# Kernel optimization log

Hardware: AMD Instinct MI355X
Metric: run time of the kernel (lower is better)

Reference implementation:

```python
import jax, jax.numpy as jnp
import numpy as np

HEADS = 8
DIM_HEAD = 64
QUERY_DIM = 512
INNER_DIM = HEADS * DIM_HEAD  # 512
SCALE = DIM_HEAD ** -0.5


def setup_inputs() -> dict:
    key = jax.random.key(0)
    k0, k1, k2, k3, k4 = jax.random.split(key, 5)
    B, S = 4, 2048
    hidden_states = jax.random.normal(k0, (B, S, QUERY_DIM), dtype=jnp.float32)
    init = lambda k, fin, fout: jax.random.normal(k, (fin, fout), dtype=jnp.float32) / np.sqrt(fin)
    return {
        "hidden_states": hidden_states,
        "Wq": init(k1, QUERY_DIM, INNER_DIM),
        "Wk": init(k2, QUERY_DIM, INNER_DIM),
        "Wv": init(k3, QUERY_DIM, INNER_DIM),
        "Wo": init(k4, INNER_DIM, QUERY_DIM),
    }


def _split_heads(x):
    # [B, S, H*D] -> [B, H, S, D]
    B, S, _ = x.shape
    return x.reshape(B, S, HEADS, DIM_HEAD).transpose(0, 2, 1, 3)


def reference(hidden_states, Wq, Wk, Wv, Wo):
    q = _split_heads(hidden_states @ Wq)
    k = _split_heads(hidden_states @ Wk)
    v = _split_heads(hidden_states @ Wv)
    # scores: [B, H, S, S]
    scores = jnp.einsum("bhid,bhjd->bhij", q, k) * SCALE
    attn = jax.nn.softmax(scores, axis=-1)
    out = jnp.einsum("bhij,bhjd->bhid", attn, v)  # [B, H, S, D]
    B, H, S, D = out.shape
    out = out.transpose(0, 2, 1, 3).reshape(B, S, H * D)
    return out @ Wo
```

## Files before the change

kernel.cpp:

```cpp
#include <hip/hip_runtime.h>
#include <hip/hip_bf16.h>

typedef __bf16 bf16;
typedef __attribute__((ext_vector_type(8))) __bf16 bf16x8;
typedef __attribute__((ext_vector_type(4))) float f32x4;

#define SEQ   2048
#define HEADS 8
#define DHEAD 64
#define CDIM  512
#define MROWS 8192
#define SCALE 0.125f

__global__ __launch_bounds__(256) void k_cvt_hs(const float* __restrict__ in,
                                                bf16* __restrict__ out) {
    int idx = blockIdx.x * 256 + threadIdx.x;
    const float4* in4 = reinterpret_cast<const float4*>(in);
    float4 a = in4[idx * 2], b = in4[idx * 2 + 1];
    bf16x8 o;
    o[0] = (bf16)a.x; o[1] = (bf16)a.y; o[2] = (bf16)a.z; o[3] = (bf16)a.w;
    o[4] = (bf16)b.x; o[5] = (bf16)b.y; o[6] = (bf16)b.z; o[7] = (bf16)b.w;
    reinterpret_cast<bf16x8*>(out)[idx] = o;
}

__global__ __launch_bounds__(256) void k_wtrans(const float* __restrict__ w0,
                                                const float* __restrict__ w1,
                                                const float* __restrict__ w2,
                                                const float* __restrict__ w3,
                                                bf16* __restrict__ wt) {
    const float* w = blockIdx.z == 0 ? w0 : blockIdx.z == 1 ? w1 : blockIdx.z == 2 ? w2 : w3;
    bf16* out = wt + (size_t)blockIdx.z * CDIM * CDIM;
    __shared__ bf16 tile[64][65];
    const int t = threadIdx.x;
    const int r0 = blockIdx.x * 64, c0 = blockIdx.y * 64;
    const int r = t >> 2, cc = (t & 3) * 16;
    const float4* src = reinterpret_cast<const float4*>(w + (size_t)(r0 + r) * CDIM + c0 + cc);
#pragma unroll
    for (int v = 0; v < 4; ++v) {
        float4 f = src[v];
        tile[r][cc + v * 4 + 0] = (bf16)f.x;
        tile[r][cc + v * 4 + 1] = (bf16)f.y;
        tile[r][cc + v * 4 + 2] = (bf16)f.z;
        tile[r][cc + v * 4 + 3] = (bf16)f.w;
    }
    __syncthreads();
    bf16x8 o0, o1;
#pragma unroll
    for (int j = 0; j < 8; ++j) { o0[j] = tile[cc + j][r]; o1[j] = tile[cc + 8 + j][r]; }
    bf16* dst = out + (size_t)(c0 + r) * CDIM + r0 + cc;
    *reinterpret_cast<bf16x8*>(dst) = o0;
    *reinterpret_cast<bf16x8*>(dst + 8) = o1;
}

__global__ __launch_bounds__(256) void k_gemm_qkv(const bf16* __restrict__ A,
                                                  const bf16* __restrict__ Wt,
                                                  bf16* __restrict__ Qb,
                                                  bf16* __restrict__ Kb,
                                                  bf16* __restrict__ Vb) {
    __shared__ __align__(16) bf16 As[128 * 32];
    __shared__ __align__(16) bf16 Bs[128 * 32];
    const int t = threadIdx.x, lane = t & 63, wid = t >> 6;
    const int wr = wid >> 1, wc = wid & 1;
    const int g = (lane >> 4) & 3, q = lane & 15;
    const int m0 = blockIdx.x * 128, n0 = blockIdx.y * 128;
    const bf16* Bmat = Wt + (size_t)blockIdx.z * CDIM * CDIM;
    f32x4 acc[4][4] = {};
    const int sr = t >> 1, sc = (t & 1) * 16;
    for (int kt = 0; kt < 16; ++kt) {
        const int k0 = kt * 32;
        const bf16x8* a_src = reinterpret_cast<const bf16x8*>(A + (size_t)(m0 + sr) * CDIM + k0 + sc);
        const bf16x8* b_src = reinterpret_cast<const bf16x8*>(Bmat + (size_t)(n0 + sr) * CDIM + k0 + sc);
        bf16x8 av0 = a_src[0], av1 = a_src[1];
        bf16x8 bv0 = b_src[0], bv1 = b_src[1];
        __syncthreads();
        *reinterpret_cast<bf16x8*>(&As[sr * 32 + sc]) = av0;
        *reinterpret_cast<bf16x8*>(&As[sr * 32 + sc + 8]) = av1;
        *reinterpret_cast<bf16x8*>(&Bs[sr * 32 + sc]) = bv0;
        *reinterpret_cast<bf16x8*>(&Bs[sr * 32 + sc + 8]) = bv1;
        __syncthreads();
        bf16x8 af[4], bfv[4];
#pragma unroll
        for (int m = 0; m < 4; ++m)
            af[m] = *reinterpret_cast<const bf16x8*>(&As[(wr * 64 + m * 16 + q) * 32 + g * 8]);
#pragma unroll
        for (int n = 0; n < 4; ++n)
            bfv[n] = *reinterpret_cast<const bf16x8*>(&Bs[(wc * 64 + n * 16 + q) * 32 + g * 8]);
#pragma unroll
        for (int m = 0; m < 4; ++m)
#pragma unroll
            for (int n = 0; n < 4; ++n)
                acc[m][n] = __builtin_amdgcn_mfma_f32_16x16x32_bf16(af[m], bfv[n], acc[m][n], 0, 0, 0);
    }
    bf16* outp = blockIdx.z == 0 ? Qb : (blockIdx.z == 1 ? Kb : Vb);
#pragma unroll
    for (int m = 0; m < 4; ++m) {
        const int rbase = m0 + wr * 64 + m * 16 + g * 4;
#pragma unroll
        for (int i = 0; i < 4; ++i) {
            const int row = rbase + i;
            const int b = row >> 11, s = row & 2047;
#pragma unroll
            for (int n = 0; n < 4; ++n) {
                const int col = n0 + wc * 64 + n * 16 + q;
                const int h = col >> 6, d = col & 63;
                outp[((((size_t)b * HEADS + h) * SEQ + s) << 6) + d] = (bf16)acc[m][n][i];
            }
        }
    }
}

__global__ __launch_bounds__(256) void k_vtrans(const bf16* __restrict__ V,
                                                bf16* __restrict__ Vt) {
    __shared__ bf16 tile[64][65];
    const int t = threadIdx.x;
    const int s0 = blockIdx.x * 64;
    const size_t bh = blockIdx.y;
    const int r = t >> 2, cc = (t & 3) * 16;
    const bf16x8* src = reinterpret_cast<const bf16x8*>(V + (bh * SEQ + s0 + r) * DHEAD + cc);
    bf16x8 v0 = src[0], v1 = src[1];
#pragma unroll
    for (int j = 0; j < 8; ++j) { tile[r][cc + j] = v0[j]; tile[r][cc + 8 + j] = v1[j]; }
    __syncthreads();
    bf16x8 o0, o1;
#pragma unroll
    for (int j = 0; j < 8; ++j) { o0[j] = tile[cc + j][r]; o1[j] = tile[cc + 8 + j][r]; }
    bf16* dst = Vt + (bh * DHEAD + r) * SEQ + s0 + cc;
    *reinterpret_cast<bf16x8*>(dst) = o0;
    *reinterpret_cast<bf16x8*>(dst + 8) = o1;
}

__global__ __launch_bounds__(256) void k_attn(const bf16* __restrict__ Qg,
                                              const bf16* __restrict__ Kg,
                                              const bf16* __restrict__ Vtg,
                                              bf16* __restrict__ Og) {
    __shared__ __align__(16) bf16 K_lds[64 * 72];
    __shared__ __align__(16) bf16 Vt_lds[64 * 72];
    __shared__ __align__(16) bf16 P_lds[4][16 * 72];
    const int t = threadIdx.x, lane = t & 63, wid = t >> 6;
    const int g = (lane >> 4) & 3, q = lane & 15;
    const size_t bh = blockIdx.y;
    const int q0 = blockIdx.x * 64 + wid * 16;
    const int b = (int)(bh >> 3), h = (int)(bh & 7);

    bf16x8 qf[2];
#pragma unroll
    for (int ks = 0; ks < 2; ++ks)
        qf[ks] = *reinterpret_cast<const bf16x8*>(Qg + (bh * SEQ + q0 + q) * DHEAD + ks * 32 + g * 8);

    f32x4 accO[4] = {};
    float m_run = -1e30f, l_run = 0.f;
    const int sr = t >> 2, scc = (t & 3) * 16;

    for (int kt = 0; kt < 32; ++kt) {
        const int kv0 = kt * 64;
        const bf16x8* ksrc = reinterpret_cast<const bf16x8*>(Kg + (bh * SEQ + kv0 + sr) * DHEAD + scc);
        const bf16x8* vsrc = reinterpret_cast<const bf16x8*>(Vtg + (bh * DHEAD + sr) * SEQ + kv0 + scc);
        bf16x8 kva = ksrc[0], kvb = ksrc[1];
        bf16x8 vva = vsrc[0], vvb = vsrc[1];
        __syncthreads();
        *reinterpret_cast<bf16x8*>(&K_lds[sr * 72 + scc]) = kva;
        *reinterpret_cast<bf16x8*>(&K_lds[sr * 72 + scc + 8]) = kvb;
        *reinterpret_cast<bf16x8*>(&Vt_lds[sr * 72 + scc]) = vva;
        *reinterpret_cast<bf16x8*>(&Vt_lds[sr * 72 + scc + 8]) = vvb;
        __syncthreads();

        f32x4 st[4] = {};
#pragma unroll
        for (int ks = 0; ks < 2; ++ks) {
            bf16x8 qk = qf[ks];
#pragma unroll
            for (int m = 0; m < 4; ++m) {
                bf16x8 kf = *reinterpret_cast<const bf16x8*>(&K_lds[(m * 16 + q) * 72 + ks * 32 + g * 8]);
                st[m] = __builtin_amdgcn_mfma_f32_16x16x32_bf16(kf, qk, st[m], 0, 0, 0);
            }
        }

        float sc[4][4];
        float tmax = -1e30f;
#pragma unroll
        for (int m = 0; m < 4; ++m)
#pragma unroll
            for (int i = 0; i < 4; ++i) {
                sc[m][i] = st[m][i] * SCALE;
                tmax = fmaxf(tmax, sc[m][i]);
            }
        tmax = fmaxf(tmax, __shfl_xor(tmax, 16));
        tmax = fmaxf(tmax, __shfl_xor(tmax, 32));
        const float mnew = fmaxf(m_run, tmax);
        const float alpha = __expf(m_run - mnew);
        float psum = 0.f;
#pragma unroll
        for (int m = 0; m < 4; ++m)
#pragma unroll
            for (int i = 0; i < 4; ++i) {
                float p = __expf(sc[m][i] - mnew);
                psum += p;
                P_lds[wid][q * 72 + m * 16 + g * 4 + i] = (bf16)p;
            }
        psum += __shfl_xor(psum, 16);
        psum += __shfl_xor(psum, 32);
        l_run = l_run * alpha + psum;
        m_run = mnew;
#pragma unroll
        for (int m = 0; m < 4; ++m)
#pragma unroll
            for (int i = 0; i < 4; ++i) accO[m][i] *= alpha;

#pragma unroll
        for (int ks = 0; ks < 2; ++ks) {
            bf16x8 pb = *reinterpret_cast<const bf16x8*>(&P_lds[wid][q * 72 + ks * 32 + g * 8]);
#pragma unroll
            for (int m = 0; m < 4; ++m) {
                bf16x8 vf = *reinterpret_cast<const bf16x8*>(&Vt_lds[(m * 16 + q) * 72 + ks * 32 + g * 8]);
                accO[m] = __builtin_amdgcn_mfma_f32_16x16x32_bf16(vf, pb, accO[m], 0, 0, 0);
            }
        }
    }

    const float inv = 1.0f / l_run;
#pragma unroll
    for (int m = 0; m < 4; ++m)
#pragma unroll
        for (int i = 0; i < 4; ++i) {
            const int d = m * 16 + g * 4 + i;
            Og[((size_t)b * SEQ + q0 + q) * (HEADS * DHEAD) + h * DHEAD + d] = (bf16)(accO[m][i] * inv);
        }
}

__global__ __launch_bounds__(256) void k_gemm_o(const bf16* __restrict__ A,
                                                const bf16* __restrict__ Bt,
                                                float* __restrict__ out) {
    __shared__ __align__(16) bf16 As[128 * 32];
    __shared__ __align__(16) bf16 Bs[128 * 32];
    const int t = threadIdx.x, lane = t & 63, wid = t >> 6;
    const int wr = wid >> 1, wc = wid & 1;
    const int g = (lane >> 4) & 3, q = lane & 15;
    const int m0 = blockIdx.x * 128, n0 = blockIdx.y * 128;
    f32x4 acc[4][4] = {};
    const int sr = t >> 1, sc = (t & 1) * 16;
    for (int kt = 0; kt < 16; ++kt) {
        const int k0 = kt * 32;
        const bf16x8* a_src = reinterpret_cast<const bf16x8*>(A + (size_t)(m0 + sr) * CDIM + k0 + sc);
        const bf16x8* b_src = reinterpret_cast<const bf16x8*>(Bt + (size_t)(n0 + sr) * CDIM + k0 + sc);
        bf16x8 av0 = a_src[0], av1 = a_src[1];
        bf16x8 bv0 = b_src[0], bv1 = b_src[1];
        __syncthreads();
        *reinterpret_cast<bf16x8*>(&As[sr * 32 + sc]) = av0;
        *reinterpret_cast<bf16x8*>(&As[sr * 32 + sc + 8]) = av1;
        *reinterpret_cast<bf16x8*>(&Bs[sr * 32 + sc]) = bv0;
        *reinterpret_cast<bf16x8*>(&Bs[sr * 32 + sc + 8]) = bv1;
        __syncthreads();
        bf16x8 af[4], bfv[4];
#pragma unroll
        for (int m = 0; m < 4; ++m)
            af[m] = *reinterpret_cast<const bf16x8*>(&As[(wr * 64 + m * 16 + q) * 32 + g * 8]);
#pragma unroll
        for (int n = 0; n < 4; ++n)
            bfv[n] = *reinterpret_cast<const bf16x8*>(&Bs[(wc * 64 + n * 16 + q) * 32 + g * 8]);
#pragma unroll
        for (int m = 0; m < 4; ++m)
#pragma unroll
            for (int n = 0; n < 4; ++n)
                acc[m][n] = __builtin_amdgcn_mfma_f32_16x16x32_bf16(af[m], bfv[n], acc[m][n], 0, 0, 0);
    }
#pragma unroll
    for (int m = 0; m < 4; ++m) {
        const int rbase = m0 + wr * 64 + m * 16 + g * 4;
#pragma unroll
        for (int i = 0; i < 4; ++i) {
            const int row = rbase + i;
#pragma unroll
            for (int n = 0; n < 4; ++n) {
                const int col = n0 + wc * 64 + n * 16 + q;
                out[(size_t)row * CDIM + col] = acc[m][n][i];
            }
        }
    }
}

extern "C" void kernel_launch(void* const* d_in, const int* in_sizes, int n_in,
                              void* d_out, int out_size, void* d_ws, size_t ws_size,
                              hipStream_t stream) {
    const float* hs = (const float*)d_in[0];
    const float* Wq = (const float*)d_in[1];
    const float* Wk = (const float*)d_in[2];
    const float* Wv = (const float*)d_in[3];
    const float* Wo = (const float*)d_in[4];
    float* out = (float*)d_out;

    bf16* hs_bf = (bf16*)d_ws;
    bf16* wt    = hs_bf + 4194304;
    bf16* Qb    = wt + 4 * 262144;
    bf16* Kb    = Qb + 4194304;
    bf16* Vb    = Kb + 4194304;
    bf16* Vt    = Vb + 4194304;
    bf16* Ob    = Vt + 4194304;

    k_cvt_hs<<<2048, 256, 0, stream>>>(hs, hs_bf);
    k_wtrans<<<dim3(8, 8, 4), 256, 0, stream>>>(Wq, Wk, Wv, Wo, wt);
    k_gemm_qkv<<<dim3(64, 4, 3), 256, 0, stream>>>(hs_bf, wt, Qb, Kb, Vb);
    k_vtrans<<<dim3(32, 32), 256, 0, stream>>>(Vb, Vt);
    k_attn<<<dim3(32, 32), 256, 0, stream>>>(Qb, Kb, Vt, Ob);
    k_gemm_o<<<dim3(64, 4), 256, 0, stream>>>(Ob, wt + 3 * 262144, out);
}
```

Measured before the change: 188.8 us.

## Rewrite QKV, attention and output kernels with async LDS loads and fragment layouts

```diff
diff --git a/kernel.cpp b/kernel.cpp
--- a/kernel.cpp
+++ b/kernel.cpp
@@ -1,16 +1,31 @@
 #include <hip/hip_runtime.h>
 #include <hip/hip_bf16.h>
+#include <stdint.h>
 
 typedef __bf16 bf16;
 typedef __attribute__((ext_vector_type(8))) __bf16 bf16x8;
 typedef __attribute__((ext_vector_type(4))) float f32x4;
+typedef __attribute__((ext_vector_type(16))) float f32x16;
 
 #define SEQ   2048
 #define HEADS 8
-#define DHEAD 64
 #define CDIM  512
-#define MROWS 8192
-#define SCALE 0.125f
+#define C2      0.18033688011112043f
+#define THR_RAW 44.3614f
+
+__device__ __forceinline__ void glds16(const bf16* g, bf16* l) {
+    __builtin_amdgcn_global_load_lds((const __attribute__((address_space(1))) void*)g,
+                                     (__attribute__((address_space(3))) void*)l, 16, 0, 0);
+}
+__device__ __forceinline__ uint32_t pk_bf16(float a, float b) {
+    uint32_t r; asm("v_cvt_pk_bf16_f32 %0, %1, %2" : "=v"(r) : "v"(a), "v"(b)); return r;
+}
+__device__ __forceinline__ void pl_swap(uint32_t &a, uint32_t &b) {
+    asm("v_permlane32_swap_b32 %0, %1" : "+v"(a), "+v"(b));
+}
+__device__ __forceinline__ void wait_vm4() { asm volatile("s_waitcnt vmcnt(4)" ::: "memory"); }
+__device__ __forceinline__ void wait_vm3() { asm volatile("s_waitcnt vmcnt(3)" ::: "memory"); }
+__device__ __forceinline__ void wait_vm0() { asm volatile("s_waitcnt vmcnt(0)" ::: "memory"); }
 
 __global__ __launch_bounds__(256) void k_cvt_hs(const float* __restrict__ in,
                                                 bf16* __restrict__ out) {
@@ -54,226 +69,262 @@
 
 __global__ __launch_bounds__(256) void k_gemm_qkv(const bf16* __restrict__ A,
                                                   const bf16* __restrict__ Wt,
-                                                  bf16* __restrict__ Qb,
-                                                  bf16* __restrict__ Kb,
-                                                  bf16* __restrict__ Vb) {
-    __shared__ __align__(16) bf16 As[128 * 32];
-    __shared__ __align__(16) bf16 Bs[128 * 32];
+                                                  bf16* __restrict__ Qg,
+                                                  bf16* __restrict__ Kf,
+                                                  bf16* __restrict__ Vf) {
+    __shared__ __align__(16) bf16 As[2][4096];
+    __shared__ __align__(16) bf16 Bs[2][4096];
+    const int id = blockIdx.x;
+    const int swz = (id & 7) * 96 + (id >> 3);
+    const int mt = swz & 63, r2 = swz >> 6;
+    const int nt = r2 & 3, z = r2 >> 2;
+    const int m0 = mt * 128, n0 = nt * 128;
     const int t = threadIdx.x, lane = t & 63, wid = t >> 6;
     const int wr = wid >> 1, wc = wid & 1;
-    const int g = (lane >> 4) & 3, q = lane & 15;
-    const int m0 = blockIdx.x * 128, n0 = blockIdx.y * 128;
-    const bf16* Bmat = Wt + (size_t)blockIdx.z * CDIM * CDIM;
+    const int q = lane & 15, g = lane >> 4;
+    const bf16* Bmat = Wt + (size_t)z * 262144;
+    const int srow = lane >> 2, scol = (lane & 3) * 8;
+
+    auto stage = [&](int buf, int kt) {
+        const int k0 = kt * 32;
+        const bf16* a0 = A + (size_t)(m0 + wid * 32 + srow) * CDIM + k0 + scol;
+        glds16(a0,             &As[buf][wid * 1024]);
+        glds16(a0 + 16 * CDIM, &As[buf][wid * 1024 + 512]);
+        const bf16* b0 = Bmat + (size_t)(n0 + wid * 32 + srow) * CDIM + k0 + scol;
+        glds16(b0,             &Bs[buf][wid * 1024]);
+        glds16(b0 + 16 * CDIM, &Bs[buf][wid * 1024 + 512]);
+    };
+
     f32x4 acc[4][4] = {};
-    const int sr = t >> 1, sc = (t & 1) * 16;
+    stage(0, 0);
     for (int kt = 0; kt < 16; ++kt) {
-        const int k0 = kt * 32;
-        const bf16x8* a_src = reinterpret_cast<const bf16x8*>(A + (size_t)(m0 + sr) * CDIM + k0 + sc);
-        const bf16x8* b_src = reinterpret_cast<const bf16x8*>(Bmat + (size_t)(n0 + sr) * CDIM + k0 + sc);
-        bf16x8 av0 = a_src[0], av1 = a_src[1];
-        bf16x8 bv0 = b_src[0], bv1 = b_src[1];
-        __syncthreads();
-        *reinterpret_cast<bf16x8*>(&As[sr * 32 + sc]) = av0;
-        *reinterpret_cast<bf16x8*>(&As[sr * 32 + sc + 8]) = av1;
-        *reinterpret_cast<bf16x8*>(&Bs[sr * 32 + sc]) = bv0;
-        *reinterpret_cast<bf16x8*>(&Bs[sr * 32 + sc + 8]) = bv1;
+        const int cur = kt & 1;
+        if (kt < 15) { stage(cur ^ 1, kt + 1); wait_vm4(); } else wait_vm0();
         __syncthreads();
         bf16x8 af[4], bfv[4];
 #pragma unroll
         for (int m = 0; m < 4; ++m)
-            af[m] = *reinterpret_cast<const bf16x8*>(&As[(wr * 64 + m * 16 + q) * 32 + g * 8]);
+            af[m] = *(const bf16x8*)&As[cur][(wr * 64 + m * 16 + q) * 32 + g * 8];
 #pragma unroll
         for (int n = 0; n < 4; ++n)
-            bfv[n] = *reinterpret_cast<const bf16x8*>(&Bs[(wc * 64 + n * 16 + q) * 32 + g * 8]);
+            bfv[n] = *(const bf16x8*)&Bs[cur][(wc * 64 + n * 16 + q) * 32 + g * 8];
 #pragma unroll
         for (int m = 0; m < 4; ++m)
 #pragma unroll
             for (int n = 0; n < 4; ++n)
-                acc[m][n] = __builtin_amdgcn_mfma_f32_16x16x32_bf16(af[m], bfv[n], acc[m][n], 0, 0, 0);
-    }
-    bf16* outp = blockIdx.z == 0 ? Qb : (blockIdx.z == 1 ? Kb : Vb);
+                acc[m][n] = __builtin_amdgcn_mfma_f32_16x16x32_bf16(bfv[n], af[m], acc[m][n], 0, 0, 0);
+        __syncthreads();
+    }
 #pragma unroll
     for (int m = 0; m < 4; ++m) {
-        const int rbase = m0 + wr * 64 + m * 16 + g * 4;
-#pragma unroll
-        for (int i = 0; i < 4; ++i) {
-            const int row = rbase + i;
-            const int b = row >> 11, s = row & 2047;
-#pragma unroll
-            for (int n = 0; n < 4; ++n) {
-                const int col = n0 + wc * 64 + n * 16 + q;
-                const int h = col >> 6, d = col & 63;
-                outp[((((size_t)b * HEADS + h) * SEQ + s) << 6) + d] = (bf16)acc[m][n][i];
+        const int row = m0 + wr * 64 + m * 16 + q;
+        const int b = row >> 11, s = row & 2047;
+#pragma unroll
+        for (int n = 0; n < 4; ++n) {
+            const int cb = n0 + wc * 64 + n * 16 + g * 4;
+            const size_t bh = (size_t)b * HEADS + (cb >> 6);
+            const int d0 = cb & 63;
+            const f32x4 v = acc[m][n];
+            if (z == 0) {
+                uint2 u; u.x = pk_bf16(v[0], v[1]); u.y = pk_bf16(v[2], v[3]);
+                *(uint2*)&Qg[(bh * SEQ + s) * 64 + d0] = u;
+            } else if (z == 1) {
+                const int tile = s >> 6, ktt = (s >> 5) & 1, l31 = s & 31;
+                const int kb = d0 >> 4, hh = (d0 >> 3) & 1, j = d0 & 7;
+                uint2 u; u.x = pk_bf16(v[0], v[1]); u.y = pk_bf16(v[2], v[3]);
+                *(uint2*)&Kf[(bh * 32 + tile) * 4096 +
+                             (size_t)(((ktt * 4 + kb) * 64 + hh * 32 + l31) * 8 + j)] = u;
+            } else {
+                const int tile = s >> 6, kvb = (s & 63) >> 4, hh = (s >> 3) & 1, jv = s & 7;
+                const int dt = d0 >> 5;
+                const size_t base = (bh * 32 + tile) * 4096;
+#pragma unroll
+                for (int i = 0; i < 4; ++i) {
+                    const int l31v = (d0 + i) & 31;
+                    Vf[base + (size_t)(((dt * 4 + kvb) * 64 + hh * 32 + l31v) * 8 + jv)] = (bf16)v[i];
+                }
             }
         }
     }
 }
 
-__global__ __launch_bounds__(256) void k_vtrans(const bf16* __restrict__ V,
-                                                bf16* __restrict__ Vt) {
-    __shared__ bf16 tile[64][65];
-    const int t = threadIdx.x;
-    const int s0 = blockIdx.x * 64;
-    const size_t bh = blockIdx.y;
-    const int r = t >> 2, cc = (t & 3) * 16;
-    const bf16x8* src = reinterpret_cast<const bf16x8*>(V + (bh * SEQ + s0 + r) * DHEAD + cc);
-    bf16x8 v0 = src[0], v1 = src[1];
-#pragma unroll
-    for (int j = 0; j < 8; ++j) { tile[r][cc + j] = v0[j]; tile[r][cc + 8 + j] = v1[j]; }
-    __syncthreads();
-    bf16x8 o0, o1;
-#pragma unroll
-    for (int j = 0; j < 8; ++j) { o0[j] = tile[cc + j][r]; o1[j] = tile[cc + 8 + j][r]; }
-    bf16* dst = Vt + (bh * DHEAD + r) * SEQ + s0 + cc;
-    *reinterpret_cast<bf16x8*>(dst) = o0;
-    *reinterpret_cast<bf16x8*>(dst + 8) = o1;
-}
-
 __global__ __launch_bounds__(256) void k_attn(const bf16* __restrict__ Qg,
-                                              const bf16* __restrict__ Kg,
-                                              const bf16* __restrict__ Vtg,
+                                              const bf16* __restrict__ Kf,
+                                              const bf16* __restrict__ Vf,
                                               bf16* __restrict__ Og) {
-    __shared__ __align__(16) bf16 K_lds[64 * 72];
-    __shared__ __align__(16) bf16 Vt_lds[64 * 72];
-    __shared__ __align__(16) bf16 P_lds[4][16 * 72];
+    __shared__ __align__(16) bf16 KV[2][2][4096];
+    const int id = blockIdx.x;
+    const int swz = (id & 7) * 64 + (id >> 3);
+    const int bh = swz >> 4, qb = swz & 15;
     const int t = threadIdx.x, lane = t & 63, wid = t >> 6;
-    const int g = (lane >> 4) & 3, q = lane & 15;
-    const size_t bh = blockIdx.y;
-    const int q0 = blockIdx.x * 64 + wid * 16;
-    const int b = (int)(bh >> 3), h = (int)(bh & 7);
-
-    bf16x8 qf[2];
-#pragma unroll
-    for (int ks = 0; ks < 2; ++ks)
-        qf[ks] = *reinterpret_cast<const bf16x8*>(Qg + (bh * SEQ + q0 + q) * DHEAD + ks * 32 + g * 8);
-
-    f32x4 accO[4] = {};
+    const int q = lane & 31, hi = lane >> 5;
+    const int q0 = qb * 128 + wid * 32;
+    const int b = bh >> 3, h = bh & 7;
+
+    bf16x8 qf[4];
+#pragma unroll
+    for (int kb = 0; kb < 4; ++kb)
+        qf[kb] = *(const bf16x8*)&Qg[((size_t)bh * SEQ + q0 + q) * 64 + kb * 16 + hi * 8];
+
+    f32x16 oacc[2] = {};
     float m_run = -1e30f, l_run = 0.f;
-    const int sr = t >> 2, scc = (t & 3) * 16;
-
+
+    auto stage = [&](int buf, int kt) {
+        const bf16* kb_ = Kf + ((size_t)bh * 32 + kt) * 4096;
+        const bf16* vb_ = Vf + ((size_t)bh * 32 + kt) * 4096;
+        const int g0 = wid * 2;
+        glds16(kb_ + g0 * 512 + lane * 8,       &KV[buf][0][g0 * 512]);
+        glds16(kb_ + (g0 + 1) * 512 + lane * 8, &KV[buf][0][(g0 + 1) * 512]);
+        glds16(vb_ + g0 * 512 + lane * 8,       &KV[buf][1][g0 * 512]);
+        glds16(vb_ + (g0 + 1) * 512 + lane * 8, &KV[buf][1][(g0 + 1) * 512]);
+    };
+
+    stage(0, 0);
     for (int kt = 0; kt < 32; ++kt) {
-        const int kv0 = kt * 64;
-        const bf16x8* ksrc = reinterpret_cast<const bf16x8*>(Kg + (bh * SEQ + kv0 + sr) * DHEAD + scc);
-        const bf16x8* vsrc = reinterpret_cast<const bf16x8*>(Vtg + (bh * DHEAD + sr) * SEQ + kv0 + scc);
-        bf16x8 kva = ksrc[0], kvb = ksrc[1];
-        bf16x8 vva = vsrc[0], vvb = vsrc[1];
-        __syncthreads();
-        *reinterpret_cast<bf16x8*>(&K_lds[sr * 72 + scc]) = kva;
-        *reinterpret_cast<bf16x8*>(&K_lds[sr * 72 + scc + 8]) = kvb;
-        *reinterpret_cast<bf16x8*>(&Vt_lds[sr * 72 + scc]) = vva;
-        *reinterpret_cast<bf16x8*>(&Vt_lds[sr * 72 + scc + 8]) = vvb;
-        __syncthreads();
-
-        f32x4 st[4] = {};
-#pragma unroll
-        for (int ks = 0; ks < 2; ++ks) {
-            bf16x8 qk = qf[ks];
-#pragma unroll
-            for (int m = 0; m < 4; ++m) {
-                bf16x8 kf = *reinterpret_cast<const bf16x8*>(&K_lds[(m * 16 + q) * 72 + ks * 32 + g * 8]);
-                st[m] = __builtin_amdgcn_mfma_f32_16x16x32_bf16(kf, qk, st[m], 0, 0, 0);
+        const int cur = kt & 1;
+        if (kt < 31) { stage(cur ^ 1, kt + 1); wait_vm4(); } else wait_vm0();
+        __syncthreads();
+
+        f32x16 sa[2] = {};
+        __builtin_amdgcn_s_setprio(1);
+#pragma unroll
+        for (int kt2 = 0; kt2 < 2; ++kt2)
+#pragma unroll
+            for (int kb = 0; kb < 4; ++kb) {
+                bf16x8 kfr = *(const bf16x8*)&KV[cur][0][((kt2 * 4 + kb) * 64 + lane) * 8];
+                sa[kt2] = __builtin_amdgcn_mfma_f32_32x32x16_bf16(kfr, qf[kb], sa[kt2], 0, 0, 0);
             }
-        }
-
-        float sc[4][4];
-        float tmax = -1e30f;
-#pragma unroll
-        for (int m = 0; m < 4; ++m)
-#pragma unroll
-            for (int i = 0; i < 4; ++i) {
-                sc[m][i] = st[m][i] * SCALE;
-                tmax = fmaxf(tmax, sc[m][i]);
+        __builtin_amdgcn_s_setprio(0);
+
+        float m8[8];
+#pragma unroll
+        for (int r = 0; r < 8; ++r)
+            m8[r] = fmaxf(fmaxf(sa[0][r], sa[0][r + 8]), fmaxf(sa[1][r], sa[1][r + 8]));
+#pragma unroll
+        for (int r = 0; r < 4; ++r) m8[r] = fmaxf(m8[r], m8[r + 4]);
+        float tmax = fmaxf(fmaxf(m8[0], m8[1]), fmaxf(m8[2], m8[3]));
+        tmax = fmaxf(tmax, __shfl_xor(tmax, 32));
+
+        if (__any(tmax > m_run + THR_RAW)) {
+            const float mnew = fmaxf(m_run, tmax);
+            const float al = exp2f((m_run - mnew) * C2);
+            l_run *= al;
+#pragma unroll
+            for (int dt = 0; dt < 2; ++dt)
+#pragma unroll
+                for (int r = 0; r < 16; ++r) oacc[dt][r] *= al;
+            m_run = mnew;
+        }
+        const float msc = m_run * C2;
+#pragma unroll
+        for (int kt2 = 0; kt2 < 2; ++kt2)
+#pragma unroll
+            for (int r = 0; r < 16; ++r)
+                sa[kt2][r] = exp2f(fmaf(sa[kt2][r], C2, -msc));
+
+        float s0 = 0.f, s1 = 0.f, s2 = 0.f, s3 = 0.f;
+#pragma unroll
+        for (int r = 0; r < 16; r += 4) {
+            s0 += sa[0][r]     + sa[1][r];
+            s1 += sa[0][r + 1] + sa[1][r + 1];
+            s2 += sa[0][r + 2] + sa[1][r + 2];
+            s3 += sa[0][r + 3] + sa[1][r + 3];
+        }
+        float psum = (s0 + s1) + (s2 + s3);
+        psum += __shfl_xor(psum, 32);
+        l_run += psum;
+
+        bf16x8 pb[4];
+#pragma unroll
+        for (int kt2 = 0; kt2 < 2; ++kt2)
+#pragma unroll
+            for (int b2 = 0; b2 < 2; ++b2) {
+                uint32_t lo0 = pk_bf16(sa[kt2][8 * b2 + 0], sa[kt2][8 * b2 + 1]);
+                uint32_t lo1 = pk_bf16(sa[kt2][8 * b2 + 2], sa[kt2][8 * b2 + 3]);
+                uint32_t hi0 = pk_bf16(sa[kt2][8 * b2 + 4], sa[kt2][8 * b2 + 5]);
+                uint32_t hi1 = pk_bf16(sa[kt2][8 * b2 + 6], sa[kt2][8 * b2 + 7]);
+                pl_swap(lo0, hi0); pl_swap(lo1, hi1);
+                union { uint32_t w[4]; bf16x8 v; } u;
+                u.w[0] = lo0; u.w[1] = lo1; u.w[2] = hi0; u.w[3] = hi1;
+                pb[kt2 * 2 + b2] = u.v;
             }
-        tmax = fmaxf(tmax, __shfl_xor(tmax, 16));
-        tmax = fmaxf(tmax, __shfl_xor(tmax, 32));
-        const float mnew = fmaxf(m_run, tmax);
-        const float alpha = __expf(m_run - mnew);
-        float psum = 0.f;
-#pragma unroll
-        for (int m = 0; m < 4; ++m)
-#pragma unroll
-            for (int i = 0; i < 4; ++i) {
-                float p = __expf(sc[m][i] - mnew);
-                psum += p;
-                P_lds[wid][q * 72 + m * 16 + g * 4 + i] = (bf16)p;
+
+        __builtin_amdgcn_s_setprio(1);
+#pragma unroll
+        for (int dt = 0; dt < 2; ++dt)
+#pragma unroll
+            for (int bb = 0; bb < 4; ++bb) {
+                bf16x8 vfr = *(const bf16x8*)&KV[cur][1][((dt * 4 + bb) * 64 + lane) * 8];
+                oacc[dt] = __builtin_amdgcn_mfma_f32_32x32x16_bf16(vfr, pb[bb], oacc[dt], 0, 0, 0);
             }
-        psum += __shfl_xor(psum, 16);
-        psum += __shfl_xor(psum, 32);
-        l_run = l_run * alpha + psum;
-        m_run = mnew;
-#pragma unroll
-        for (int m = 0; m < 4; ++m)
-#pragma unroll
-            for (int i = 0; i < 4; ++i) accO[m][i] *= alpha;
-
-#pragma unroll
-        for (int ks = 0; ks < 2; ++ks) {
-            bf16x8 pb = *reinterpret_cast<const bf16x8*>(&P_lds[wid][q * 72 + ks * 32 + g * 8]);
-#pragma unroll
-            for (int m = 0; m < 4; ++m) {
-                bf16x8 vf = *reinterpret_cast<const bf16x8*>(&Vt_lds[(m * 16 + q) * 72 + ks * 32 + g * 8]);
-                accO[m] = __builtin_amdgcn_mfma_f32_16x16x32_bf16(vf, pb, accO[m], 0, 0, 0);
-            }
-        }
+        __builtin_amdgcn_s_setprio(0);
+        __syncthreads();
     }
 
     const float inv = 1.0f / l_run;
-#pragma unroll
-    for (int m = 0; m < 4; ++m)
-#pragma unroll
-        for (int i = 0; i < 4; ++i) {
-            const int d = m * 16 + g * 4 + i;
-            Og[((size_t)b * SEQ + q0 + q) * (HEADS * DHEAD) + h * DHEAD + d] = (bf16)(accO[m][i] * inv);
+    bf16* orow = Og + ((size_t)b * SEQ + q0 + q) * CDIM + h * 64;
+#pragma unroll
+    for (int dt = 0; dt < 2; ++dt)
+#pragma unroll
+        for (int rr = 0; rr < 4; ++rr) {
+            const int d0 = dt * 32 + rr * 8 + hi * 4;
+            uint2 u;
+            u.x = pk_bf16(oacc[dt][4 * rr] * inv,     oacc[dt][4 * rr + 1] * inv);
+            u.y = pk_bf16(oacc[dt][4 * rr + 2] * inv, oacc[dt][4 * rr + 3] * inv);
+            *(uint2*)&orow[d0] = u;
         }
 }
 
 __global__ __launch_bounds__(256) void k_gemm_o(const bf16* __restrict__ A,
                                                 const bf16* __restrict__ Bt,
                                                 float* __restrict__ out) {
-    __shared__ __align__(16) bf16 As[128 * 32];
-    __shared__ __align__(16) bf16 Bs[128 * 32];
+    __shared__ __align__(16) bf16 As[2][4096];
+    __shared__ __align__(16) bf16 Bs[2][2048];
+    const int id = blockIdx.x;
+    const int swz = (id & 7) * 64 + (id >> 3);
+    const int mt = swz & 63, nt = swz >> 6;
+    const int m0 = mt * 128, n0 = nt * 64;
     const int t = threadIdx.x, lane = t & 63, wid = t >> 6;
     const int wr = wid >> 1, wc = wid & 1;
-    const int g = (lane >> 4) & 3, q = lane & 15;
-    const int m0 = blockIdx.x * 128, n0 = blockIdx.y * 128;
-    f32x4 acc[4][4] = {};
-    const int sr = t >> 1, sc = (t & 1) * 16;
+    const int q = lane & 15, g = lane >> 4;
+    const int srow = lane >> 2, scol = (lane & 3) * 8;
+
+    auto stage = [&](int buf, int kt) {
+        const int k0 = kt * 32;
+        const bf16* a0 = A + (size_t)(m0 + wid * 32 + srow) * CDIM + k0 + scol;
+        glds16(a0,             &As[buf][wid * 1024]);
+        glds16(a0 + 16 * CDIM, &As[buf][wid * 1024 + 512]);
+        const bf16* b0 = Bt + (size_t)(n0 + wid * 16 + srow) * CDIM + k0 + scol;
+        glds16(b0, &Bs[buf][wid * 512]);
+    };
+
+    f32x4 acc[4][2] = {};
+    stage(0, 0);
     for (int kt = 0; kt < 16; ++kt) {
-        const int k0 = kt * 32;
-        const bf16x8* a_src = reinterpret_cast<const bf16x8*>(A + (size_t)(m0 + sr) * CDIM + k0 + sc);
-        const bf16x8* b_src = reinterpret_cast<const bf16x8*>(Bt + (size_t)(n0 + sr) * CDIM + k0 + sc);
-        bf16x8 av0 = a_src[0], av1 = a_src[1];
-        bf16x8 bv0 = b_src[0], bv1 = b_src[1];
-        __syncthreads();
-        *reinterpret_cast<bf16x8*>(&As[sr * 32 + sc]) = av0;
-        *reinterpret_cast<bf16x8*>(&As[sr * 32 + sc + 8]) = av1;
-        *reinterpret_cast<bf16x8*>(&Bs[sr * 32 + sc]) = bv0;
-        *reinterpret_cast<bf16x8*>(&Bs[sr * 32 + sc + 8]) = bv1;
-        __syncthreads();
-        bf16x8 af[4], bfv[4];
+        const int cur = kt & 1;
+        if (kt < 15) { stage(cur ^ 1, kt + 1); wait_vm3(); } else wait_vm0();
+        __syncthreads();
+        bf16x8 af[4], bfv[2];
 #pragma unroll
         for (int m = 0; m < 4; ++m)
-            af[m] = *reinterpret_cast<const bf16x8*>(&As[(wr * 64 + m * 16 + q) * 32 + g * 8]);
-#pragma unroll
-        for (int n = 0; n < 4; ++n)
-            bfv[n] = *reinterpret_cast<const bf16x8*>(&Bs[(wc * 64 + n * 16 + q) * 32 + g * 8]);
+            af[m] = *(const bf16x8*)&As[cur][(wr * 64 + m * 16 + q) * 32 + g * 8];
+#pragma unroll
+        for (int n = 0; n < 2; ++n)
+            bfv[n] = *(const bf16x8*)&Bs[cur][(wc * 32 + n * 16 + q) * 32 + g * 8];
 #pragma unroll
         for (int m = 0; m < 4; ++m)
 #pragma unroll
-            for (int n = 0; n < 4; ++n)
-                acc[m][n] = __builtin_amdgcn_mfma_f32_16x16x32_bf16(af[m], bfv[n], acc[m][n], 0, 0, 0);
+            for (int n = 0; n < 2; ++n)
+                acc[m][n] = __builtin_amdgcn_mfma_f32_16x16x32_bf16(bfv[n], af[m], acc[m][n], 0, 0, 0);
+        __syncthreads();
     }
 #pragma unroll
     for (int m = 0; m < 4; ++m) {
-        const int rbase = m0 + wr * 64 + m * 16 + g * 4;
-#pragma unroll
-        for (int i = 0; i < 4; ++i) {
-            const int row = rbase + i;
-#pragma unroll
-            for (int n = 0; n < 4; ++n) {
-                const int col = n0 + wc * 64 + n * 16 + q;
-                out[(size_t)row * CDIM + col] = acc[m][n][i];
-            }
+        const int row = m0 + wr * 64 + m * 16 + q;
+#pragma unroll
+        for (int n = 0; n < 2; ++n) {
+            const int cb = n0 + wc * 32 + n * 16 + g * 4;
+            *(f32x4*)&out[(size_t)row * CDIM + cb] = acc[m][n];
         }
     }
 }
@@ -290,16 +341,14 @@
 
     bf16* hs_bf = (bf16*)d_ws;
     bf16* wt    = hs_bf + 4194304;
-    bf16* Qb    = wt + 4 * 262144;
-    bf16* Kb    = Qb + 4194304;
-    bf16* Vb    = Kb + 4194304;
-    bf16* Vt    = Vb + 4194304;
-    bf16* Ob    = Vt + 4194304;
+    bf16* Qg    = wt + 1048576;
+    bf16* Kf    = Qg + 4194304;
+    bf16* Vf    = Kf + 4194304;
+    bf16* Og    = Vf + 4194304;
 
     k_cvt_hs<<<2048, 256, 0, stream>>>(hs, hs_bf);
     k_wtrans<<<dim3(8, 8, 4), 256, 0, stream>>>(Wq, Wk, Wv, Wo, wt);
-    k_gemm_qkv<<<dim3(64, 4, 3), 256, 0, stream>>>(hs_bf, wt, Qb, Kb, Vb);
-    k_vtrans<<<dim3(32, 32), 256, 0, stream>>>(Vb, Vt);
-    k_attn<<<dim3(32, 32), 256, 0, stream>>>(Qb, Kb, Vt, Ob);
-    k_gemm_o<<<dim3(64, 4), 256, 0, stream>>>(Ob, wt + 3 * 262144, out);
-}
+    k_gemm_qkv<<<768, 256, 0, stream>>>(hs_bf, wt, Qg, Kf, Vf);
+    k_attn<<<512, 256, 0, stream>>>(Qg, Kf, Vf, Og);
+    k_gemm_o<<<512, 256, 0, stream>>>(Og, wt + 3 * 262144, out);
+}
```

Result: no change. 191.4 us (+1.4%).
